# Optimization experiments

Hardware: AMD Instinct MI355X
Metric: run time of the kernel (lower is better)

## Reference

```python
import jax, jax.numpy as jnp
import numpy as np

B, T, V, E, H = 512, 512, 50000, 100, 40


def gru_dir(x, lens, Wih, Whh, bih, bhh, reverse):
    """One GRU direction with length masking (PyTorch gate math).
    x: [B,T,I]; returns (out [B,T,H] zero-padded past lens, h_last [B,H])."""
    Bx, Tx, _ = x.shape
    Hh = Whh.shape[1]
    # precompute input-side gates: [T,B,3H]
    gx = jnp.einsum('bti,gi->tbg', x, Wih) + bih
    valid = (jnp.arange(Tx)[:, None] < lens[None, :])[..., None]  # [T,B,1]

    def step(h, inputs):
        gx_t, v = inputs
        gh = h @ Whh.T + bhh
        r = jax.nn.sigmoid(gx_t[:, :Hh] + gh[:, :Hh])
        z = jax.nn.sigmoid(gx_t[:, Hh:2 * Hh] + gh[:, Hh:2 * Hh])
        n = jnp.tanh(gx_t[:, 2 * Hh:] + r * gh[:, 2 * Hh:])
        hn = (1.0 - z) * n + z * h
        h = jnp.where(v, hn, h)          # freeze state past valid length
        return h, jnp.where(v, hn, 0.0)  # pad_packed_sequence zero-fills

    h0 = jnp.zeros((Bx, Hh), x.dtype)
    h_last, outs = jax.lax.scan(step, h0, (gx, valid), reverse=reverse)
    return jnp.transpose(outs, (1, 0, 2)), h_last


def setup_inputs() -> dict:
    key = jax.random.key(0)
    ks = jax.random.split(key, 24)
    text_len = jax.random.randint(ks[0], (B,), 1, T + 1)
    text = jax.random.randint(ks[1], (B, T), 1, V)
    text = jnp.where(jnp.arange(T)[None, :] < text_len[:, None], text, 0)
    s = 0.1
    emb = jax.random.normal(ks[2], (V, E), jnp.float32) * s
    emb = emb.at[0].set(0.0)  # padding_idx=0
    def mk(k, shape):
        return jax.random.normal(k, shape, jnp.float32) * s
    inp = {
        'text': text, 'text_len': text_len, 'emb': emb,
        'Wih0f': mk(ks[3], (3 * H, E)), 'Whh0f': mk(ks[4], (3 * H, H)),
        'bih0f': mk(ks[5], (3 * H,)), 'bhh0f': mk(ks[6], (3 * H,)),
        'Wih0b': mk(ks[7], (3 * H, E)), 'Whh0b': mk(ks[8], (3 * H, H)),
        'bih0b': mk(ks[9], (3 * H,)), 'bhh0b': mk(ks[10], (3 * H,)),
        'Wih1f': mk(ks[11], (3 * H, 2 * H)), 'Whh1f': mk(ks[12], (3 * H, H)),
        'bih1f': mk(ks[13], (3 * H,)), 'bhh1f': mk(ks[14], (3 * H,)),
        'Wih1b': mk(ks[15], (3 * H, 2 * H)), 'Whh1b': mk(ks[16], (3 * H, H)),
        'bih1b': mk(ks[17], (3 * H,)), 'bhh1b': mk(ks[18], (3 * H,)),
        'fc1_W': mk(ks[19], (128, 8 * H)), 'fc1_b': mk(ks[20], (128,)),
        'fc2_W': mk(ks[21], (1, 128)), 'fc2_b': mk(ks[22], (1,)),
    }
    return inp


def forward(text, text_len, emb, Wih0f, Whh0f, bih0f, bhh0f, Wih0b, Whh0b, bih0b, bhh0b,
            Wih1f, Whh1f, bih1f, bhh1f, Wih1b, Whh1b, bih1b, bhh1b,
            fc1_W, fc1_b, fc2_W, fc2_b):
    x = emb[text]  # [B,T,E]
    # layer 0 (bidirectional)
    of0, hf0 = gru_dir(x, text_len, Wih0f, Whh0f, bih0f, bhh0f, False)
    ob0, hb0 = gru_dir(x, text_len, Wih0b, Whh0b, bih0b, bhh0b, True)
    x1 = jnp.concatenate([of0, ob0], axis=-1)  # [B,T,2H]; inter-layer dropout is eval no-op
    # layer 1 (bidirectional)
    of1, hf1 = gru_dir(x1, text_len, Wih1f, Whh1f, bih1f, bhh1f, False)
    ob1, hb1 = gru_dir(x1, text_len, Wih1b, Whh1b, bih1b, bhh1b, True)
    out = jnp.concatenate([of1, ob1], axis=-1)  # [B,T,2H], zero past lens
    # masked avg / max pooling over valid timesteps
    avg_pool = jnp.sum(out, axis=1) / text_len[:, None].astype(out.dtype)
    valid = (jnp.arange(T)[None, :] < text_len[:, None])[..., None]  # [B,T,1]
    max_pool = jnp.max(jnp.where(valid, out, -jnp.inf), axis=1)
    # hidden order: [l0_fwd, l0_bwd, l1_fwd, l1_bwd]; cat([-1],[-2],[-3],[-4],...)
    pool_cat = jnp.concatenate([hb1, hf1, hb0, hf0, avg_pool, max_pool], axis=1)  # [B,8H]
    h = pool_cat @ fc1_W.T + fc1_b
    h = jnp.where(h >= 0, h, 0.01 * h)  # leaky_relu (dropouts are eval no-ops)
    return h @ fc2_W.T + fc2_b  # [B,1]


def reference(text, text_len, emb, Wih0f, Whh0f, bih0f, bhh0f, Wih0b, Whh0b, bih0b, bhh0b,
              Wih1f, Whh1f, bih1f, bhh1f, Wih1b, Whh1b, bih1b, bhh1b,
              fc1_W, fc1_b, fc2_W, fc2_b):
    return forward(text, text_len, emb, Wih0f, Whh0f, bih0f, bhh0f, Wih0b, Whh0b, bih0b, bhh0b,
                   Wih1f, Whh1f, bih1f, bhh1f, Wih1b, Whh1b, bih1b, bhh1b,
                   fc1_W, fc1_b, fc2_W, fc2_b)
```

## Files before the change

kernel.cpp:

```cpp
#include <hip/hip_runtime.h>
#include <hip/hip_fp16.h>

#define BB 512
#define TT 512
#define EE 100
#define HH 40
#define GG 120
#define TC 64
#define NC 8
#define X1S 96

typedef _Float16 h2_t __attribute__((ext_vector_type(2)));
typedef _Float16 h8_t __attribute__((ext_vector_type(8)));
typedef float    f4_t __attribute__((ext_vector_type(4)));

__device__ __forceinline__ float fdot2_(h2_t a, h2_t b, float c) {
    return __builtin_amdgcn_fdot2(a, b, c, false);
}
__device__ __forceinline__ h2_t pack2_(float x, float y) {
    h2_t r; r[0] = (_Float16)x; r[1] = (_Float16)y; return r;
}
__device__ __forceinline__ float sigmoid_(float x) {
    return __builtin_amdgcn_rcpf(1.0f + __expf(-x));
}
__device__ __forceinline__ float tanhfast_(float x) {
    return 1.0f - 2.0f * __builtin_amdgcn_rcpf(__expf(2.0f * x) + 1.0f);
}

template<int K, bool GATHER>
__global__ __launch_bounds__(256, 2) void fused_kernel(
    const int cg, const int cs, const int nScan,
    const int* __restrict__ text, const __half* __restrict__ emb16,
    const __half* __restrict__ Xh,
    const _Float16* __restrict__ Wt,
    const float* __restrict__ bf, const float* __restrict__ bb,
    __half* __restrict__ gxW, const __half* __restrict__ gxR,
    const _Float16* __restrict__ WhhL,
    const float* __restrict__ bhhF, const float* __restrict__ bhhB,
    const int* __restrict__ lens,
    __half* __restrict__ out0,
    float* __restrict__ hcar, float* __restrict__ hlast,
    float* __restrict__ sumb, float* __restrict__ maxb)
{
    constexpr int KS = (K == 100) ? 4 : 3;
    __shared__ __align__(16) _Float16 hsh[4][48];
    const int tid = threadIdx.x;

    if ((int)blockIdx.x < nScan) {
        __builtin_amdgcn_s_setprio(3);
        const int wave = tid >> 6, j = tid & 63;
        if (j >= HH) return;
        const int chain = blockIdx.x * 4 + wave;
        const int dir = chain >> 9;
        const int b   = chain & (BB - 1);
        const float* bhh = dir ? bhhB : bhhF;

        h8_t R0,R1,R2,R3,R4, Z0,Z1,Z2,Z3,Z4, N0,N1,N2,N3,N4;
        {
            const _Float16* wr = WhhL + (size_t)dir * 4800;
            const h8_t* pr = (const h8_t*)(wr + (size_t)j * 40);
            const h8_t* pz = (const h8_t*)(wr + (size_t)(40 + j) * 40);
            const h8_t* pn = (const h8_t*)(wr + (size_t)(80 + j) * 40);
            R0=pr[0]; R1=pr[1]; R2=pr[2]; R3=pr[3]; R4=pr[4];
            Z0=pz[0]; Z1=pz[1]; Z2=pz[2]; Z3=pz[3]; Z4=pz[4];
            N0=pn[0]; N1=pn[1]; N2=pn[2]; N3=pn[3]; N4=pn[4];
        }
        asm volatile("" : "+v"(R0),"+v"(R1),"+v"(R2),"+v"(R3),"+v"(R4),
                          "+v"(Z0),"+v"(Z1),"+v"(Z2),"+v"(Z3),"+v"(Z4),
                          "+v"(N0),"+v"(N1),"+v"(N2),"+v"(N3),"+v"(N4));
        const float br = bhh[j], bz = bhh[HH + j], bn = bhh[2*HH + j];
        const int len = lens[b];
        const int chunk = dir ? (NC - 1 - cs) : cs;
        const int tbase = chunk * TC;

        int sBeg, sEnd;
        if (dir == 0) { sBeg = 0; sEnd = min(TC, max(0, len - tbase)); }
        else          { sBeg = max(0, tbase + TC - len); sEnd = TC; }

        float h = (cs == 0) ? 0.0f : hcar[(size_t)(dir * BB + b) * HH + j];
        hsh[wave][j] = (_Float16)h;
        float psum = 0.0f, pmax = -3.4e38f;
        const size_t gxRow = ((size_t)dir * BB + b) * TC;
        const float4* h4 = (const float4*)hsh[wave];

        struct G3 { __half r, z, n; };
        auto ldg3 = [&](int sc) -> G3 {
            const int tl = dir ? (TC - 1 - sc) : sc;
            const __half* gp = gxR + (gxRow + tl) * GG;
            G3 g; g.r = gp[j]; g.z = gp[HH + j]; g.n = gp[2*HH + j];
            return g;
        };
#define SL(V,i) __builtin_shufflevector(V, V, 2*(i), 2*(i)+1)
#define DOTQ(Rq,Zq,Nq,U) \
        r0 = fdot2_(SL(Rq,0), U.hh[0], r0); \
        z0 = fdot2_(SL(Zq,0), U.hh[0], z0); \
        n0 = fdot2_(SL(Nq,0), U.hh[0], n0); \
        r1 = fdot2_(SL(Rq,1), U.hh[1], r1); \
        z1 = fdot2_(SL(Zq,1), U.hh[1], z1); \
        n1 = fdot2_(SL(Nq,1), U.hh[1], n1); \
        r0 = fdot2_(SL(Rq,2), U.hh[2], r0); \
        z0 = fdot2_(SL(Zq,2), U.hh[2], z0); \
        n0 = fdot2_(SL(Nq,2), U.hh[2], n0); \
        r1 = fdot2_(SL(Rq,3), U.hh[3], r1); \
        z1 = fdot2_(SL(Zq,3), U.hh[3], z1); \
        n1 = fdot2_(SL(Nq,3), U.hh[3], n1);

        constexpr int PF = 4;
        auto step = [&](int s, G3& g, bool pf) {
            G3 nx;
            if (pf) nx = ldg3(min(s + PF, sEnd - 1));
            const int tloc = dir ? (TC - 1 - s) : s;
            float r0 = br, r1 = 0.f, z0 = bz, z1 = 0.f, n0 = bn, n1 = 0.f;
            union { float4 f; h2_t hh[4]; } u0, u1, u2, u3, u4;
            u0.f = h4[0]; u1.f = h4[1]; u2.f = h4[2]; u3.f = h4[3]; u4.f = h4[4];
            DOTQ(R0,Z0,N0,u0)
            DOTQ(R1,Z1,N1,u1)
            DOTQ(R2,Z2,N2,u2)
            DOTQ(R3,Z3,N3,u3)
            DOTQ(R4,Z4,N4,u4)
            const float rr = sigmoid_(__half2float(g.r) + r0 + r1);
            const float zz = sigmoid_(__half2float(g.z) + z0 + z1);
            const float nn = tanhfast_(__half2float(g.n) + rr * (n0 + n1));
            const float hn = (1.0f - zz) * nn + zz * h;
            h = hn;
            hsh[wave][j] = (_Float16)h;
            if (GATHER) {
                const int t = tbase + tloc;
                out0[((size_t)b * TT + t) * X1S + dir*HH + j] = __float2half(hn);
            } else {
                psum += hn;
                pmax = fmaxf(pmax, hn);
            }
            if (pf) g = nx;
        };

        G3 q0 = {}, q1 = {}, q2 = {}, q3 = {};
        if (sBeg < sEnd) {
            q0 = ldg3(sBeg);
            q1 = ldg3(min(sBeg + 1, sEnd - 1));
            q2 = ldg3(min(sBeg + 2, sEnd - 1));
            q3 = ldg3(min(sBeg + 3, sEnd - 1));
        }
        int s = sBeg;
        for (; s + PF <= sEnd; s += PF) {
            step(s + 0, q0, true);
            step(s + 1, q1, true);
            step(s + 2, q2, true);
            step(s + 3, q3, true);
        }
        if (s     < sEnd) step(s,     q0, false);
        if (s + 1 < sEnd) step(s + 1, q1, false);
        if (s + 2 < sEnd) step(s + 2, q2, false);

        hcar[(size_t)(dir * BB + b) * HH + j] = h;
        const int layer = GATHER ? 0 : 1;
        if (cs == NC - 1)
            hlast[((size_t)(layer * 2 + dir) * BB + b) * HH + j] = h;
        if (!GATHER) {
            const size_t pi = (size_t)b * (2*HH) + dir*HH + j;
            if (cs == 0) { sumb[pi] = psum;  maxb[pi] = pmax; }
            else         { sumb[pi] += psum; maxb[pi] = fmaxf(maxb[pi], pmax); }
        }
        return;
    }

    __builtin_amdgcn_s_setprio(0);
    const int gid = blockIdx.x - nScan;
    const int b   = gid & (BB - 1);
    const int dir = gid >> 9;
    const int chunk = dir ? (NC - 1 - cg) : cg;
    const int tbase = chunk * TC;
    if (tbase >= lens[b]) return;
    const float* bias = dir ? bb : bf;
    const _Float16* Wg = Wt + (size_t)dir * (KS * 8 * 64 * 8);

    const int w = tid >> 6, l = tid & 63;
    const int row = l & 15, kq = l >> 4;
    const int t0 = tbase + w * 16 + row;
    h8_t A[4];
    if (GATHER) {
        const int tok = text[b * TT + t0];
        const _Float16* ap = (const _Float16*)emb16 + (size_t)tok * 128 + kq * 8;
        #pragma unroll
        for (int ks = 0; ks < KS; ++ks) A[ks] = *(const h8_t*)(ap + ks * 32);
    } else {
        const _Float16* ap = (const _Float16*)Xh + ((size_t)b * TT + t0) * X1S + kq * 8;
        #pragma unroll
        for (int ks = 0; ks < KS; ++ks) A[ks] = *(const h8_t*)(ap + ks * 32);
    }

    f4_t acc[8] = {};
    #pragma unroll
    for (int ks = 0; ks < KS; ++ks)
        #pragma unroll
        for (int f = 0; f < 8; ++f) {
            const h8_t Bf = *(const h8_t*)(Wg + ((size_t)(ks * 8 + f) * 64 + l) * 8);
            acc[f] = __builtin_amdgcn_mfma_f32_16x16x32_f16(A[ks], Bf, acc[f], 0, 0, 0);
        }

    const size_t rowB = ((size_t)dir * BB + b) * TC;
    const int gb = l & 15, rq = l >> 4;
    #pragma unroll
    for (int f = 0; f < 8; ++f) {
        const int gate = f * 16 + gb;
        if (gate < GG) {
            const float bv = bias[gate];
            #pragma unroll
            for (int r = 0; r < 4; ++r) {
                const int tloc = w * 16 + rq * 4 + r;
                gxW[(rowB + tloc) * GG + gate] = __float2half(acc[f][r] + bv);
            }
        }
    }
}

#define NE2 (50000 * 64)
#define NW0 (2*4*8*64)
#define NW1 (2*3*8*64)
#define NHH (4*120*20)
#define NP0 (BB*TT*8)
__global__ __launch_bounds__(256) void prep_kernel(
    const float* __restrict__ emb,
    const float* __restrict__ Wih0f, const float* __restrict__ Wih0b,
    const float* __restrict__ Wih1f, const float* __restrict__ Wih1b,
    const float* __restrict__ Whh0f, const float* __restrict__ Whh0b,
    const float* __restrict__ Whh1f, const float* __restrict__ Whh1b,
    __half* __restrict__ emb16, _Float16* __restrict__ Wt16,
    _Float16* __restrict__ Whh16, __half* __restrict__ out0)
{
    const int gid = blockIdx.x * 256 + threadIdx.x;
    if (gid < NE2) {
        const int v = gid >> 6, q2 = gid & 63;
        const int k0 = q2 * 2;
        float x0 = 0.f, x1 = 0.f;
        if (k0 < EE) { x0 = emb[(size_t)v * EE + k0]; x1 = emb[(size_t)v * EE + k0 + 1]; }
        ((h2_t*)emb16)[(size_t)v * 64 + q2] = pack2_(x0, x1);
        return;
    }
    int e = gid - NE2;
    if (e < NP0) {
        const int row = e >> 3, q = e & 7;
        ((h2_t*)out0)[(size_t)row * 48 + 40 + q] = pack2_(0.f, 0.f);
        return;
    }
    e -= NP0;
    if (e < NW0) {
        const int l = e & 63, f = (e >> 6) & 7, ks = (e >> 9) & 3, dir = e >> 11;
        const float* W = dir ? Wih0b : Wih0f;
        const int col = f * 16 + (l & 15);
        const int kb  = ks * 32 + (l >> 4) * 8;
        _Float16* dst = Wt16 + (size_t)e * 8;
        #pragma unroll
        for (int i = 0; i < 8; ++i) {
            const int k = kb + i;
            dst[i] = (_Float16)((col < GG && k < EE) ? W[(size_t)col * EE + k] : 0.f);
        }
        return;
    }
    e -= NW0;
    if (e < NW1) {
        const int l = e & 63, f = (e >> 6) & 7;
        const int t = e >> 9;
        const int ks = t % 3, dir = t / 3;
        const float* W = dir ? Wih1b : Wih1f;
        const int col = f * 16 + (l & 15);
        const int kb  = ks * 32 + (l >> 4) * 8;
        _Float16* dst = Wt16 + (size_t)(NW0 + e) * 8;
        #pragma unroll
        for (int i = 0; i < 8; ++i) {
            const int k = kb + i;
            dst[i] = (_Float16)((col < GG && k < 2*HH) ? W[(size_t)col * (2*HH) + k] : 0.f);
        }
        return;
    }
    e -= NW1;
    if (e < NHH) {
        const int ld = e / 2400, rem = e - ld * 2400;
        const int row2 = rem / 20, kk = rem - row2 * 20;
        const float* W = (ld == 0) ? Whh0f : (ld == 1) ? Whh0b
                       : (ld == 2) ? Whh1f : Whh1b;
        ((h2_t*)Whh16)[e] = pack2_(W[row2*HH + 2*kk], W[row2*HH + 2*kk + 1]);
    }
}

__global__ __launch_bounds__(128) void fc_kernel(
    const float* __restrict__ hlast, const float* __restrict__ sumb,
    const float* __restrict__ maxb, const int* __restrict__ lens,
    const float* __restrict__ fc1W, const float* __restrict__ fc1b,
    const float* __restrict__ fc2W, const float* __restrict__ fc2b,
    float* __restrict__ out)
{
    __shared__ float pool[8 * HH];
    __shared__ float red[128];
    const int b = blockIdx.x, tid = threadIdx.x;
    if (tid < HH) {
        pool[tid]        = hlast[(size_t)(3*BB + b) * HH + tid];
        pool[HH + tid]   = hlast[(size_t)(2*BB + b) * HH + tid];
        pool[2*HH + tid] = hlast[(size_t)(1*BB + b) * HH + tid];
        pool[3*HH + tid] = hlast[(size_t)(0*BB + b) * HH + tid];
    }
    const float invLen = 1.0f / (float)lens[b];
    if (tid < 2*HH) {
        pool[4*HH + tid] = sumb[(size_t)b * 2*HH + tid] * invLen;
        pool[6*HH + tid] = maxb[(size_t)b * 2*HH + tid];
    }
    __syncthreads();
    float acc = fc1b[tid];
    for (int k = 0; k < 8*HH; ++k)
        acc = fmaf(pool[k], fc1W[(size_t)tid * (8*HH) + k], acc);
    float v = (acc >= 0.0f) ? acc : 0.01f * acc;
    red[tid] = v * fc2W[tid];
    __syncthreads();
    for (int s = 64; s > 0; s >>= 1) {
        if (tid < s) red[tid] += red[tid + s];
        __syncthreads();
    }
    if (tid == 0) out[b] = red[0] + fc2b[0];
}

extern "C" void kernel_launch(void* const* d_in, const int* in_sizes, int n_in,
                              void* d_out, int out_size, void* d_ws, size_t ws_size,
                              hipStream_t stream) {
    const int*   text  = (const int*)d_in[0];
    const int*   lens  = (const int*)d_in[1];
    const float* emb   = (const float*)d_in[2];
    const float* Wih0f = (const float*)d_in[3];
    const float* Whh0f = (const float*)d_in[4];
    const float* bih0f = (const float*)d_in[5];
    const float* bhh0f = (const float*)d_in[6];
    const float* Wih0b = (const float*)d_in[7];
    const float* Whh0b = (const float*)d_in[8];
    const float* bih0b = (const float*)d_in[9];
    const float* bhh0b = (const float*)d_in[10];
    const float* Wih1f = (const float*)d_in[11];
    const float* Whh1f = (const float*)d_in[12];
    const float* bih1f = (const float*)d_in[13];
    const float* bhh1f = (const float*)d_in[14];
    const float* Wih1b = (const float*)d_in[15];
    const float* Whh1b = (const float*)d_in[16];
    const float* bih1b = (const float*)d_in[17];
    const float* bhh1b = (const float*)d_in[18];
    const float* fc1W  = (const float*)d_in[19];
    const float* fc1b  = (const float*)d_in[20];
    const float* fc2W  = (const float*)d_in[21];
    const float* fc2b  = (const float*)d_in[22];
    float* out = (float*)d_out;

    char* p = (char*)d_ws;
    const size_t gxB = (size_t)2 * BB * TC * GG * sizeof(__half);
    __half* gxb0  = (__half*)p;  p += gxB;
    __half* gxb1  = (__half*)p;  p += gxB;
    __half* out0  = (__half*)p;  p += (size_t)BB * TT * X1S * sizeof(__half);
    float*  hcar  = (float*)p;   p += (size_t)2 * BB * HH * sizeof(float);
    float*  hlast = (float*)p;   p += (size_t)4 * BB * HH * sizeof(float);
    float*  sumb  = (float*)p;   p += (size_t)BB * 2 * HH * sizeof(float);
    float*  maxb  = (float*)p;   p += (size_t)BB * 2 * HH * sizeof(float);
    __half*    emb16 = (__half*)p;    p += (size_t)50000 * 128 * sizeof(__half);
    _Float16*  Wt16  = (_Float16*)p;  p += (size_t)(NW0 + NW1) * 8 * sizeof(_Float16);
    _Float16*  Whh16 = (_Float16*)p;
    __half* gxb[2] = { gxb0, gxb1 };

    const int NG = BB * 2;
    const int NS = 256;

    {
        const int total = NE2 + NP0 + NW0 + NW1 + NHH;
        prep_kernel<<<(total + 255) / 256, 256, 0, stream>>>(
            emb, Wih0f, Wih0b, Wih1f, Wih1b, Whh0f, Whh0b, Whh1f, Whh1b,
            emb16, Wt16, Whh16, out0);
    }

    fused_kernel<EE, true><<<NG, 256, 0, stream>>>(0, 0, 0,
        text, emb16, nullptr, Wt16, bih0f, bih0b,
        gxb[0], gxb[0], Whh16, bhh0f, bhh0b,
        lens, out0, hcar, hlast, sumb, maxb);
    for (int ci = 1; ci < NC; ++ci)
        fused_kernel<EE, true><<<NS + NG, 256, 0, stream>>>(ci, ci - 1, NS,
            text, emb16, nullptr, Wt16, bih0f, bih0b,
            gxb[ci & 1], gxb[(ci - 1) & 1], Whh16, bhh0f, bhh0b,
            lens, out0, hcar, hlast, sumb, maxb);
    fused_kernel<EE, true><<<NS, 256, 0, stream>>>(0, NC - 1, NS,
        text, emb16, nullptr, Wt16, bih0f, bih0b,
        gxb[0], gxb[(NC - 1) & 1], Whh16, bhh0f, bhh0b,
        lens, out0, hcar, hlast, sumb, maxb);

    fused_kernel<2*HH, false><<<NG, 256, 0, stream>>>(0, 0, 0,
        text, emb16, out0, Wt16 + (size_t)NW0 * 8, bih1f, bih1b,
        gxb[0], gxb[0], Whh16 + 9600, bhh1f, bhh1b,
        lens, out0, hcar, hlast, sumb, maxb);
    for (int ci = 1; ci < NC; ++ci)
        fused_kernel<2*HH, false><<<NS + NG, 256, 0, stream>>>(ci, ci - 1, NS,
            text, emb16, out0, Wt16 + (size_t)NW0 * 8, bih1f, bih1b,
            gxb[ci & 1], gxb[(ci - 1) & 1], Whh16 + 9600, bhh1f, bhh1b,
            lens, out0, hcar, hlast, sumb, maxb);
    fused_kernel<2*HH, false><<<NS, 256, 0, stream>>>(0, NC - 1, NS,
        text, emb16, out0, Wt16 + (size_t)NW0 * 8, bih1f, bih1b,
        gxb[0], gxb[(NC - 1) & 1], Whh16 + 9600, bhh1f, bhh1b,
        lens, out0, hcar, hlast, sumb, maxb);

    fc_kernel<<<BB, 128, 0, stream>>>(hlast, sumb, maxb, lens,
        fc1W, fc1b, fc2W, fc2b, out);
}
```

Before: 572.3 us.

## Interleave two batch chains per scan wave to hide recurrence latency

Each scan wave now advances two independent GRU chains (batch b and b+256) in interleaved steps, each with its own shared-memory hidden-state row, and the number of scan blocks is halved. The goal is to fill the dependent-latency gaps of the serial recurrence (dot products, shared-memory round trip, transcendentals) with independent work from the second chain. In exchange, per-wave register pressure rises, each chain's serial length grows with the interleave, and the prefetch depth drops from four to two steps.

```diff
diff --git a/kernel.cpp b/kernel.cpp
--- a/kernel.cpp
+++ b/kernel.cpp
@@ -43,16 +43,17 @@
     float* __restrict__ sumb, float* __restrict__ maxb)
 {
     constexpr int KS = (K == 100) ? 4 : 3;
-    __shared__ __align__(16) _Float16 hsh[4][48];
+    __shared__ __align__(16) _Float16 hsh[4][2][48];
     const int tid = threadIdx.x;
 
     if ((int)blockIdx.x < nScan) {
         __builtin_amdgcn_s_setprio(3);
         const int wave = tid >> 6, j = tid & 63;
         if (j >= HH) return;
-        const int chain = blockIdx.x * 4 + wave;
-        const int dir = chain >> 9;
-        const int b   = chain & (BB - 1);
+        const int p   = blockIdx.x * 4 + wave;
+        const int dir = p >> 8;
+        const int bA  = p & 255;
+        const int bB  = bA + 256;
         const float* bhh = dir ? bhhB : bhhF;
 
         h8_t R0,R1,R2,R3,R4, Z0,Z1,Z2,Z3,Z4, N0,N1,N2,N3,N4;
@@ -69,23 +70,33 @@
                           "+v"(Z0),"+v"(Z1),"+v"(Z2),"+v"(Z3),"+v"(Z4),
                           "+v"(N0),"+v"(N1),"+v"(N2),"+v"(N3),"+v"(N4));
         const float br = bhh[j], bz = bhh[HH + j], bn = bhh[2*HH + j];
-        const int len = lens[b];
         const int chunk = dir ? (NC - 1 - cs) : cs;
         const int tbase = chunk * TC;
 
-        int sBeg, sEnd;
-        if (dir == 0) { sBeg = 0; sEnd = min(TC, max(0, len - tbase)); }
-        else          { sBeg = max(0, tbase + TC - len); sEnd = TC; }
-
-        float h = (cs == 0) ? 0.0f : hcar[(size_t)(dir * BB + b) * HH + j];
-        hsh[wave][j] = (_Float16)h;
-        float psum = 0.0f, pmax = -3.4e38f;
-        const size_t gxRow = ((size_t)dir * BB + b) * TC;
-        const float4* h4 = (const float4*)hsh[wave];
+        const int lenA = lens[bA], lenB = lens[bB];
+        int sBegA, sEndA, sBegB, sEndB;
+        if (dir == 0) {
+            sBegA = 0; sEndA = min(TC, max(0, lenA - tbase));
+            sBegB = 0; sEndB = min(TC, max(0, lenB - tbase));
+        } else {
+            sBegA = max(0, tbase + TC - lenA); sEndA = TC;
+            sBegB = max(0, tbase + TC - lenB); sEndB = TC;
+        }
+
+        float hA = (cs == 0) ? 0.0f : hcar[(size_t)(dir * BB + bA) * HH + j];
+        float hB = (cs == 0) ? 0.0f : hcar[(size_t)(dir * BB + bB) * HH + j];
+        hsh[wave][0][j] = (_Float16)hA;
+        hsh[wave][1][j] = (_Float16)hB;
+        float psA = 0.0f, pmA = -3.4e38f, psB = 0.0f, pmB = -3.4e38f;
+        const size_t gxRowA = ((size_t)dir * BB + bA) * TC;
+        const size_t gxRowB = ((size_t)dir * BB + bB) * TC;
+        const float4* h4A = (const float4*)hsh[wave][0];
+        const float4* h4B = (const float4*)hsh[wave][1];
 
         struct G3 { __half r, z, n; };
-        auto ldg3 = [&](int sc) -> G3 {
-            const int tl = dir ? (TC - 1 - sc) : sc;
+        auto ldg3 = [&](size_t gxRow, int sc, int sEnd) -> G3 {
+            const int scc = max(0, min(sc, sEnd - 1));
+            const int tl = dir ? (TC - 1 - scc) : scc;
             const __half* gp = gxR + (gxRow + tl) * GG;
             G3 g; g.r = gp[j]; g.z = gp[HH + j]; g.n = gp[2*HH + j];
             return g;
@@ -105,10 +116,8 @@
         z1 = fdot2_(SL(Zq,3), U.hh[3], z1); \
         n1 = fdot2_(SL(Nq,3), U.hh[3], n1);
 
-        constexpr int PF = 4;
-        auto step = [&](int s, G3& g, bool pf) {
-            G3 nx;
-            if (pf) nx = ldg3(min(s + PF, sEnd - 1));
+        auto stepX = [&](int s, G3 g, float& h, _Float16* hrow,
+                         const float4* h4, int bX, float& psum, float& pmax) {
             const int tloc = dir ? (TC - 1 - s) : s;
             float r0 = br, r1 = 0.f, z0 = bz, z1 = 0.f, n0 = bn, n1 = 0.f;
             union { float4 f; h2_t hh[4]; } u0, u1, u2, u3, u4;
@@ -123,43 +132,60 @@
             const float nn = tanhfast_(__half2float(g.n) + rr * (n0 + n1));
             const float hn = (1.0f - zz) * nn + zz * h;
             h = hn;
-            hsh[wave][j] = (_Float16)h;
+            hrow[j] = (_Float16)hn;
             if (GATHER) {
                 const int t = tbase + tloc;
-                out0[((size_t)b * TT + t) * X1S + dir*HH + j] = __float2half(hn);
+                out0[((size_t)bX * TT + t) * X1S + dir*HH + j] = __float2half(hn);
             } else {
                 psum += hn;
                 pmax = fmaxf(pmax, hn);
             }
-            if (pf) g = nx;
         };
 
-        G3 q0 = {}, q1 = {}, q2 = {}, q3 = {};
-        if (sBeg < sEnd) {
-            q0 = ldg3(sBeg);
-            q1 = ldg3(min(sBeg + 1, sEnd - 1));
-            q2 = ldg3(min(sBeg + 2, sEnd - 1));
-            q3 = ldg3(min(sBeg + 3, sEnd - 1));
-        }
-        int s = sBeg;
-        for (; s + PF <= sEnd; s += PF) {
-            step(s + 0, q0, true);
-            step(s + 1, q1, true);
-            step(s + 2, q2, true);
-            step(s + 3, q3, true);
-        }
-        if (s     < sEnd) step(s,     q0, false);
-        if (s + 1 < sEnd) step(s + 1, q1, false);
-        if (s + 2 < sEnd) step(s + 2, q2, false);
-
-        hcar[(size_t)(dir * BB + b) * HH + j] = h;
+        const int s0 = min(sBegA, sBegB);
+        const int s1 = max(sEndA, sEndB);
+        G3 a0 = ldg3(gxRowA, s0,     sEndA);
+        G3 a1 = ldg3(gxRowA, s0 + 1, sEndA);
+        G3 b0 = ldg3(gxRowB, s0,     sEndB);
+        G3 b1 = ldg3(gxRowB, s0 + 1, sEndB);
+        int s = s0;
+        for (; s + 2 <= s1; s += 2) {
+            G3 na = ldg3(gxRowA, s + 2, sEndA);
+            G3 nb = ldg3(gxRowB, s + 2, sEndB);
+            if (s >= sBegA && s < sEndA)
+                stepX(s, a0, hA, hsh[wave][0], h4A, bA, psA, pmA);
+            if (s >= sBegB && s < sEndB)
+                stepX(s, b0, hB, hsh[wave][1], h4B, bB, psB, pmB);
+            a0 = na; b0 = nb;
+            na = ldg3(gxRowA, s + 3, sEndA);
+            nb = ldg3(gxRowB, s + 3, sEndB);
+            if (s + 1 >= sBegA && s + 1 < sEndA)
+                stepX(s + 1, a1, hA, hsh[wave][0], h4A, bA, psA, pmA);
+            if (s + 1 >= sBegB && s + 1 < sEndB)
+                stepX(s + 1, b1, hB, hsh[wave][1], h4B, bB, psB, pmB);
+            a1 = na; b1 = nb;
+        }
+        if (s < s1) {
+            if (s >= sBegA && s < sEndA)
+                stepX(s, a0, hA, hsh[wave][0], h4A, bA, psA, pmA);
+            if (s >= sBegB && s < sEndB)
+                stepX(s, b0, hB, hsh[wave][1], h4B, bB, psB, pmB);
+        }
+
+        hcar[(size_t)(dir * BB + bA) * HH + j] = hA;
+        hcar[(size_t)(dir * BB + bB) * HH + j] = hB;
         const int layer = GATHER ? 0 : 1;
-        if (cs == NC - 1)
-            hlast[((size_t)(layer * 2 + dir) * BB + b) * HH + j] = h;
+        if (cs == NC - 1) {
+            hlast[((size_t)(layer * 2 + dir) * BB + bA) * HH + j] = hA;
+            hlast[((size_t)(layer * 2 + dir) * BB + bB) * HH + j] = hB;
+        }
         if (!GATHER) {
-            const size_t pi = (size_t)b * (2*HH) + dir*HH + j;
-            if (cs == 0) { sumb[pi] = psum;  maxb[pi] = pmax; }
-            else         { sumb[pi] += psum; maxb[pi] = fmaxf(maxb[pi], pmax); }
+            const size_t piA = (size_t)bA * (2*HH) + dir*HH + j;
+            const size_t piB = (size_t)bB * (2*HH) + dir*HH + j;
+            if (cs == 0) { sumb[piA] = psA;  maxb[piA] = pmA;
+                           sumb[piB] = psB;  maxb[piB] = pmB; }
+            else         { sumb[piA] += psA; maxb[piA] = fmaxf(maxb[piA], pmA);
+                           sumb[piB] += psB; maxb[piB] = fmaxf(maxb[piB], pmB); }
         }
         return;
     }
@@ -361,7 +387,7 @@
     __half* gxb[2] = { gxb0, gxb1 };
 
     const int NG = BB * 2;
-    const int NS = 256;
+    const int NS = 128;
 
     {
         const int total = NE2 + NP0 + NW0 + NW1 + NHH;
```

After: 825.2 us. +44.2%, slower.
